# Kernel optimization log

Measured on AMD Instinct MI355X. Metric: run time of the kernel, lower is better.

## Reference

```python
import jax, jax.numpy as jnp
import numpy as np

D_MODEL = 1024
NUM_HEADS = 16
HEAD_DIM = D_MODEL // NUM_HEADS
B, S = 2, 2048


def setup_inputs() -> dict:
    key = jax.random.key(0)
    ks = jax.random.split(key, 10)
    sc = 1.0 / np.sqrt(D_MODEL)
    return {
        "x": jax.random.normal(ks[0], (B, S, D_MODEL), jnp.float32),
        "y": jax.random.normal(ks[1], (B, S, D_MODEL), jnp.float32),
        "Wkv": jax.random.normal(ks[2], (D_MODEL, 2 * D_MODEL), jnp.float32) * sc,
        "bkv": jax.random.normal(ks[3], (2 * D_MODEL,), jnp.float32) * 0.01,
        "Wq": jax.random.normal(ks[4], (D_MODEL, D_MODEL), jnp.float32) * sc,
        "bq": jax.random.normal(ks[5], (D_MODEL,), jnp.float32) * 0.01,
        "Wo": jax.random.normal(ks[6], (D_MODEL, D_MODEL), jnp.float32) * sc,
        "bo": jax.random.normal(ks[7], (D_MODEL,), jnp.float32) * 0.01,
    }


def reference(x, y, Wkv, bkv, Wq, bq, Wo, bo):
    b, s, d = x.shape
    # projections: kv from x (keys/values come from encoder side), q from y
    kv = x @ Wkv + bkv                      # [B, S, 2*d_model]
    q = y @ Wq + bq                         # [B, S, d_model]
    kv = kv.reshape(b, s, NUM_HEADS, 2 * HEAD_DIM).transpose(0, 2, 1, 3)  # [B,H,S,2*hd]
    q = q.reshape(b, s, NUM_HEADS, HEAD_DIM).transpose(0, 2, 1, 3)        # [B,H,S,hd]
    k, v = jnp.split(kv, 2, axis=-1)        # each [B,H,S,hd]
    scaled = jnp.einsum("bhqd,bhkd->bhqk", q, k) / np.sqrt(HEAD_DIM)      # [B,H,S,S]
    attention = jax.nn.softmax(scaled, axis=-1)
    values = jnp.einsum("bhqk,bhkd->bhqd", attention, v)                  # [B,H,S,hd]
    values = values.transpose(0, 2, 1, 3).reshape(b, s, d)                # [B,S,d_model]
    return values @ Wo + bo
```

## Files before the change

kernel.cpp:

```cpp
#include <hip/hip_runtime.h>
#include <hip/hip_bf16.h>

typedef __attribute__((ext_vector_type(8))) short short8;
typedef __attribute__((ext_vector_type(4))) short short4v;
typedef __attribute__((ext_vector_type(4))) float f32x4;

#define B_  2
#define S_  2048
#define H_  16
#define HD_ 64
#define D_  1024
#define QSCALE 0.18033688f

__device__ __forceinline__ short f2bs(float f) {
  union { float f; unsigned u; } c; c.f = f;
  unsigned u = c.u;
  u += 0x7fffu + ((u >> 16) & 1u);
  return (short)(u >> 16);
}

__device__ __forceinline__ float bs2f(short v) {
  union { unsigned u; float f; } c;
  c.u = ((unsigned)(unsigned short)v) << 16;
  return c.f;
}

__device__ __forceinline__ unsigned pack_bf16(float a, float b) {
  __hip_bfloat162 h = __float22bfloat162_rn(float2{a, b});
  return *reinterpret_cast<unsigned*>(&h);
}

__device__ __forceinline__ float fexp2(float x) {
#if __has_builtin(__builtin_amdgcn_exp2f)
  return __builtin_amdgcn_exp2f(x);
#else
  return exp2f(x);
#endif
}

__device__ __forceinline__ float frcp(float x) {
#if __has_builtin(__builtin_amdgcn_rcpf)
  return __builtin_amdgcn_rcpf(x);
#else
  return 1.0f / x;
#endif
}

#define GL2LDS(gp, lp) __builtin_amdgcn_global_load_lds( \
    (const __attribute__((address_space(1))) unsigned int*)(gp), \
    (__attribute__((address_space(3))) unsigned int*)(lp), 16, 0, 0)

__global__ __launch_bounds__(256)
void prep_kernel(const float* __restrict__ x, const float* __restrict__ y,
                 short* __restrict__ xb, short* __restrict__ yb,
                 const float* __restrict__ Wkv, short* __restrict__ Wkvt,
                 const float* __restrict__ Wq, short* __restrict__ Wqt,
                 const float* __restrict__ Wo, short* __restrict__ Wot) {
  __shared__ float tile[64][65];
  int bx = blockIdx.x;
  if (bx < 8192) {
    int i = bx * 256 + threadIdx.x;
    const float4* src; short4v* dst; int j;
    if (i < (1 << 20)) { src = (const float4*)x; dst = (short4v*)xb; j = i; }
    else               { src = (const float4*)y; dst = (short4v*)yb; j = i - (1 << 20); }
    float4 f = src[j];
    short4v o;
    o.x = f2bs(f.x); o.y = f2bs(f.y); o.z = f2bs(f.z); o.w = f2bs(f.w);
    dst[j] = o;
    return;
  }
  bx -= 8192;
  const float* in; short* out; int C, c0, r0;
  if (bx < 512)      { in = Wkv; out = Wkvt; C = 2048; c0 = (bx & 31) * 64; r0 = (bx >> 5) * 64; }
  else if (bx < 768) { bx -= 512; in = Wq; out = Wqt; C = 1024; c0 = (bx & 15) * 64; r0 = (bx >> 4) * 64; }
  else               { bx -= 768; in = Wo; out = Wot; C = 1024; c0 = (bx & 15) * 64; r0 = (bx >> 4) * 64; }
  const int tx = threadIdx.x & 63, ty = threadIdx.x >> 6;
#pragma unroll
  for (int i = 0; i < 16; ++i) {
    int r = ty + i * 4;
    tile[r][tx] = in[(size_t)(r0 + r) * C + c0 + tx];
  }
  __syncthreads();
#pragma unroll
  for (int i = 0; i < 16; ++i) {
    int r = ty + i * 4;
    out[(size_t)(c0 + r) * 1024 + r0 + tx] = f2bs(tile[tx][r]);
  }
}

template <int MODE>
__device__ __forceinline__ void gemm_body(const short* __restrict__ A, const short* __restrict__ Bt,
                                          const float* __restrict__ bias,
                                          void* __restrict__ out0, void* __restrict__ out1,
                                          int m0, int n0, int K, short* smem) {
  short* As = smem;
  short* Bs = smem + 4096;
  const int tid = threadIdx.x;
  const int w = tid >> 6, lane = tid & 63;
  const int q15 = lane & 15, quad = lane >> 4;
  const int wm = (w >> 1) * 64, wn = (w & 1) * 64;

  f32x4 acc[4][4];
#pragma unroll
  for (int i = 0; i < 4; ++i)
#pragma unroll
    for (int j = 0; j < 4; ++j) acc[i][j] = f32x4{0.f, 0.f, 0.f, 0.f};

  const int srow = w * 16 + (lane >> 2);
  const int gch  = (lane & 3) ^ ((lane >> 3) & 3);
  const short* Ag = A + (size_t)(m0 + srow) * K + gch * 8;
  const short* Bg = Bt + (size_t)(n0 + srow) * K + gch * 8;
  short* Al = As + srow * 32 + (lane & 3) * 8;
  short* Bl = Bs + srow * 32 + (lane & 3) * 8;

  for (int kt = 0; kt < K; kt += 32) {
    GL2LDS(Ag + kt,                  Al);
    GL2LDS(Ag + kt + (size_t)64 * K, Al + 64 * 32);
    GL2LDS(Bg + kt,                  Bl);
    GL2LDS(Bg + kt + (size_t)64 * K, Bl + 64 * 32);
    __syncthreads();
    short8 af[4], bf[4];
#pragma unroll
    for (int mi = 0; mi < 4; ++mi) {
      int rr = wm + mi * 16 + q15;
      af[mi] = *(const short8*)(As + rr * 32 + ((quad ^ ((rr >> 1) & 3)) * 8));
    }
#pragma unroll
    for (int ni = 0; ni < 4; ++ni) {
      int rr = wn + ni * 16 + q15;
      bf[ni] = *(const short8*)(Bs + rr * 32 + ((quad ^ ((rr >> 1) & 3)) * 8));
    }
#pragma unroll
    for (int mi = 0; mi < 4; ++mi)
#pragma unroll
      for (int ni = 0; ni < 4; ++ni)
        acc[mi][ni] = __builtin_amdgcn_mfma_f32_16x16x32_bf16(af[mi], bf[ni], acc[mi][ni], 0, 0, 0);
    __syncthreads();
  }

  if constexpr (MODE == 0) {
#pragma unroll
    for (int mi = 0; mi < 4; ++mi)
#pragma unroll
      for (int ni = 0; ni < 4; ++ni) {
        const int n = n0 + wn + ni * 16 + q15;
        const float bn = bias[n];
#pragma unroll
        for (int r = 0; r < 4; ++r) {
          const int m = m0 + wm + mi * 16 + quad * 4 + r;
          int b = m >> 11, s = m & 2047, hh = n >> 6, d = n & 63;
          ((short*)out0)[((size_t)((b * H_ + hh) * S_ + s) << 6) + d] = f2bs((acc[mi][ni][r] + bn) * QSCALE);
        }
      }
  } else {
    const int hh = n0 >> 7;
    const int bb = m0 >> 11;
    const size_t bh = (size_t)(bb * H_ + hh);
    const int s0 = m0 & 2047;
    if ((w & 1) == 0) {
#pragma unroll
      for (int mi = 0; mi < 4; ++mi)
#pragma unroll
        for (int ni = 0; ni < 4; ++ni) {
          const float bn = bias[n0 + ni * 16 + q15];
#pragma unroll
          for (int r = 0; r < 4; ++r) {
            const int s = s0 + wm + mi * 16 + quad * 4 + r;
            ((short*)out0)[((bh * S_ + s) << 6) + ni * 16 + q15] = f2bs(acc[mi][ni][r] + bn);
          }
        }
    } else {
      short* VT = smem;
#pragma unroll
      for (int mi = 0; mi < 4; ++mi)
#pragma unroll
        for (int ni = 0; ni < 4; ++ni) {
          const int d = ni * 16 + q15;
          const float bn = bias[n0 + 64 + ni * 16 + q15];
#pragma unroll
          for (int t = 0; t < 2; ++t) {
            const int chunk = (wm >> 1) + mi * 8 + quad * 2 + t;
            unsigned pk = pack_bf16(acc[mi][ni][2 * t] + bn, acc[mi][ni][2 * t + 1] + bn);
            *reinterpret_cast<unsigned*>(VT + d * 128 + ((chunk ^ (d & 15)) * 2)) = pk;
          }
        }
    }
    __syncthreads();
    {
      short* VT = smem;
      const int d = tid >> 2, t4 = tid & 3;
      unsigned vals[16];
#pragma unroll
      for (int c = 0; c < 16; ++c) {
        int chunk = t4 * 16 + c;
        vals[c] = *reinterpret_cast<unsigned*>(VT + d * 128 + ((chunk ^ (d & 15)) * 2));
      }
      uint4* dst = (uint4*)((short*)out1 + ((bh * HD_ + d) << 11) + s0 + t4 * 32);
      dst[0] = uint4{vals[0], vals[1], vals[2], vals[3]};
      dst[1] = uint4{vals[4], vals[5], vals[6], vals[7]};
      dst[2] = uint4{vals[8], vals[9], vals[10], vals[11]};
      dst[3] = uint4{vals[12], vals[13], vals[14], vals[15]};
    }
  }
}

__global__ __launch_bounds__(256)
void proj_kernel(const short* __restrict__ xb, const short* __restrict__ Wkvt,
                 const float* __restrict__ bkv, short* __restrict__ Kb, short* __restrict__ Vtb,
                 const short* __restrict__ yb, const short* __restrict__ Wqt,
                 const float* __restrict__ bq, short* __restrict__ Qb) {
  __shared__ __align__(16) short smem[8192];
  int bx = blockIdx.x;
  if (bx < 512)
    gemm_body<1>(xb, Wkvt, bkv, Kb, Vtb, (bx >> 4) * 128, (bx & 15) * 128, 1024, smem);
  else {
    bx -= 512;
    gemm_body<0>(yb, Wqt, bq, Qb, nullptr, (bx >> 3) * 128, (bx & 7) * 128, 1024, smem);
  }
}

__global__ __launch_bounds__(512, 4)
void gemm_o_kernel(const short* __restrict__ A, const short* __restrict__ Bt,
                   const float* __restrict__ bias, float* __restrict__ out) {
  __shared__ __align__(16) short lds[32768];
  const int tid = threadIdx.x;
  const int w = tid >> 6, lane = tid & 63;
  const int q15 = lane & 15, quad = lane >> 4;
  const int xw = q15 & 7;
  const int m0 = blockIdx.y * 128, n0 = blockIdx.x * 128;
  const int wr = (w >> 1) * 32, wc = (w & 1) * 64;

  f32x4 acc[2][4];
#pragma unroll
  for (int i = 0; i < 2; ++i)
#pragma unroll
    for (int j = 0; j < 4; ++j) acc[i][j] = f32x4{0.f, 0.f, 0.f, 0.f};

  const int srow = w * 8 + (lane >> 3);
  const int gch  = (lane & 7) ^ (srow & 7);
  const int loff = w * 512 + lane * 8;
  const short* Ag = A + (size_t)(m0 + srow) * 1024 + gch * 8;
  const short* Bg = Bt + (size_t)(n0 + srow) * 1024 + gch * 8;

  GL2LDS(Ag,             lds + loff);
  GL2LDS(Ag + 64 * 1024, lds + loff + 4096);
  GL2LDS(Bg,             lds + 16384 + loff);
  GL2LDS(Bg + 64 * 1024, lds + 16384 + loff + 4096);

  for (int kt = 0; kt < 16; ++kt) {
    __syncthreads();
    const short* Ac = lds + ((kt & 1) ? 8192 : 0);
    const short* Bc = lds + 16384 + ((kt & 1) ? 8192 : 0);
    if (kt < 15) {
      const short* a2 = Ag + (kt + 1) * 64;
      const short* b2 = Bg + (kt + 1) * 64;
      short* ad = lds + ((kt & 1) ? 0 : 8192) + loff;
      short* bd = lds + 16384 + ((kt & 1) ? 0 : 8192) + loff;
      GL2LDS(a2,             ad);
      GL2LDS(a2 + 64 * 1024, ad + 4096);
      GL2LDS(b2,             bd);
      GL2LDS(b2 + 64 * 1024, bd + 4096);
    }
    short8 af[2][2], bf[4][2];
#pragma unroll
    for (int mi = 0; mi < 2; ++mi)
#pragma unroll
      for (int kk = 0; kk < 2; ++kk)
        af[mi][kk] = *(const short8*)(Ac + (wr + mi * 16 + q15) * 64 + (((kk * 4 + quad) ^ xw) * 8));
#pragma unroll
    for (int ni = 0; ni < 4; ++ni)
#pragma unroll
      for (int kk = 0; kk < 2; ++kk)
        bf[ni][kk] = *(const short8*)(Bc + (wc + ni * 16 + q15) * 64 + (((kk * 4 + quad) ^ xw) * 8));
#pragma unroll
    for (int mi = 0; mi < 2; ++mi)
#pragma unroll
      for (int ni = 0; ni < 4; ++ni)
#pragma unroll
        for (int kk = 0; kk < 2; ++kk)
          acc[mi][ni] = __builtin_amdgcn_mfma_f32_16x16x32_bf16(af[mi][kk], bf[ni][kk], acc[mi][ni], 0, 0, 0);
  }

#pragma unroll
  for (int mi = 0; mi < 2; ++mi)
#pragma unroll
    for (int ni = 0; ni < 4; ++ni) {
      const int n = n0 + wc + ni * 16 + q15;
      const float bn = bias[n];
#pragma unroll
      for (int r = 0; r < 4; ++r) {
        const int m = m0 + wr + mi * 16 + quad * 4 + r;
        out[(size_t)m * 1024 + n] = acc[mi][ni][r] + bn;
      }
    }
}

__global__ __launch_bounds__(256, 2)
void attn_kernel(const short* __restrict__ Q, const short* __restrict__ K,
                 const short* __restrict__ Vt, short* __restrict__ Obase,
                 float* __restrict__ Ls) {
  __shared__ __align__(16) short lds[32768];
  short* PQ = lds + 16384;
  const int tid = threadIdx.x;
  const int w = tid >> 6, lane = tid & 63;
  const int q15 = lane & 15, quad = lane >> 4;
  const int xw = q15 & 7;
  const int bx = blockIdx.x;
  const int xcd = bx & 7, slot = bx >> 3;
  const int pg = slot >> 4, rest = slot & 15;
  const int half = rest >> 3, qt = rest & 7;
  const int pp = xcd * 4 + pg;
  const int h = pp & 15, b = pp >> 4;
  const size_t bh = (size_t)(b * H_ + h);
  const short* Qg = Q + bh * (S_ * HD_) + qt * (256 * HD_);
  const short* Kg = K + bh * (S_ * HD_);
  const short* Vg = Vt + bh * (HD_ * S_);

  const int srow = w * 8 + (lane >> 3);
  const int gch  = (lane & 7) ^ (srow & 7);
  const int loff = w * 512 + lane * 8;

  {
    const short* qg = Qg + srow * 64 + gch * 8;
#pragma unroll
    for (int t = 0; t < 8; ++t) GL2LDS(qg + t * 2048, PQ + loff + t * 2048);
  }
  const short* kg = Kg + srow * 64 + gch * 8;
  const short* vg = Vg + (size_t)srow * S_ + gch * 8;
  const int kt0 = half * 16;
  GL2LDS(kg + kt0 * 4096,          lds + loff);
  GL2LDS(kg + kt0 * 4096 + 2048,   lds + loff + 2048);
  GL2LDS(vg + kt0 * 64,                    lds + 8192 + loff);
  GL2LDS(vg + kt0 * 64 + (size_t)32 * S_,  lds + 8192 + loff + 2048);
  __syncthreads();

  short8 aq[4][2];
#pragma unroll
  for (int st = 0; st < 4; ++st)
#pragma unroll
    for (int kk = 0; kk < 2; ++kk)
      aq[st][kk] = *(const short8*)(PQ + (w * 64 + st * 16 + q15) * 64 + (((kk * 4 + quad) ^ xw) * 8));
  short* Psw = PQ + w * 4096;

  f32x4 oacc[4][4];
#pragma unroll
  for (int st = 0; st < 4; ++st)
#pragma unroll
    for (int ni = 0; ni < 4; ++ni) oacc[st][ni] = f32x4{0.f, 0.f, 0.f, 0.f};
  float lsum[4] = {0.f, 0.f, 0.f, 0.f};
  const f32x4 zz = {0.f, 0.f, 0.f, 0.f};

  for (int kt = 0; kt < 16; ++kt) {
    __syncthreads();
    const short* Kc = lds + ((kt & 1) ? 4096 : 0);
    const short* Vc = lds + 8192 + ((kt & 1) ? 4096 : 0);
    if (kt < 15) {
      const int kn = kt0 + kt + 1;
      short* kd = lds + ((kt & 1) ? 0 : 4096) + loff;
      short* vd = lds + 8192 + ((kt & 1) ? 0 : 4096) + loff;
      GL2LDS(kg + kn * 4096,          kd);
      GL2LDS(kg + kn * 4096 + 2048,   kd + 2048);
      GL2LDS(vg + kn * 64,                    vd);
      GL2LDS(vg + kn * 64 + (size_t)32 * S_,  vd + 2048);
    }

    short8 ka[4][2];
#pragma unroll
    for (int mi = 0; mi < 4; ++mi) {
      const short* kr = Kc + (mi * 16 + q15) * 64;
      ka[mi][0] = *(const short8*)(kr + ((quad ^ xw) * 8));
      ka[mi][1] = *(const short8*)(kr + (((quad + 4) ^ xw) * 8));
    }

#pragma unroll
    for (int st = 0; st < 4; ++st) {
      short* Pst = Psw + st * 1024;
#pragma unroll
      for (int mi = 0; mi < 4; ++mi) {
        f32x4 t = __builtin_amdgcn_mfma_f32_16x16x32_bf16(ka[mi][0], aq[st][0], zz, 0, 0, 0);
        f32x4 s = __builtin_amdgcn_mfma_f32_16x16x32_bf16(ka[mi][1], aq[st][1], t, 0, 0, 0);
        float p0 = fexp2(s[0]), p1 = fexp2(s[1]), p2 = fexp2(s[2]), p3 = fexp2(s[3]);
        lsum[st] += (p0 + p1) + (p2 + p3);
        uint2 pk;
        pk.x = pack_bf16(p0, p1);
        pk.y = pack_bf16(p2, p3);
        *reinterpret_cast<uint2*>(Pst + q15 * 64 + (((mi * 2 + (quad >> 1)) ^ xw) * 8) + (quad & 1) * 4) = pk;
      }
    }

    short8 ap[4][2];
#pragma unroll
    for (int st = 0; st < 4; ++st)
#pragma unroll
      for (int kk = 0; kk < 2; ++kk)
        ap[st][kk] = *(const short8*)(Psw + st * 1024 + q15 * 64 + (((kk * 4 + quad) ^ xw) * 8));
#pragma unroll
    for (int ni = 0; ni < 4; ++ni) {
      const short* vr = Vc + (ni * 16 + q15) * 64;
#pragma unroll
      for (int kk = 0; kk < 2; ++kk) {
        short8 bv = *(const short8*)(vr + (((kk * 4 + quad) ^ xw) * 8));
#pragma unroll
        for (int st = 0; st < 4; ++st)
          oacc[st][ni] = __builtin_amdgcn_mfma_f32_16x16x32_bf16(ap[st][kk], bv, oacc[st][ni], 0, 0, 0);
      }
    }
  }

  short* Op = Obase + (size_t)half * (4 << 20);
#pragma unroll
  for (int st = 0; st < 4; ++st) {
    float l = lsum[st];
    l += __shfl_xor(l, 16);
    l += __shfl_xor(l, 32);
    const int qrow = qt * 256 + w * 64 + st * 16;
    if (quad == 0)
      Ls[half * 65536 + (int)bh * 2048 + qrow + q15] = l;
#pragma unroll
    for (int ni = 0; ni < 4; ++ni) {
      const int col = h * HD_ + ni * 16 + q15;
#pragma unroll
      for (int r = 0; r < 4; ++r) {
        const int m = b * S_ + qrow + quad * 4 + r;
        Op[(size_t)m * D_ + col] = f2bs(oacc[st][ni][r]);
      }
    }
  }
}

__global__ __launch_bounds__(256)
void comb_kernel(const short* __restrict__ O0, const short* __restrict__ O1,
                 const float* __restrict__ Ls, short* __restrict__ AO) {
  int idx = blockIdx.x * 256 + threadIdx.x;
  int m = idx >> 7, seg = idx & 127;
  int b = m >> 11, s = m & 2047, h = seg >> 3;
  int li = (b * 16 + h) * 2048 + s;
  float inv = frcp(Ls[li] + Ls[65536 + li]);
  short8 a = *(const short8*)(O0 + (size_t)m * 1024 + seg * 8);
  short8 c = *(const short8*)(O1 + (size_t)m * 1024 + seg * 8);
  short8 o;
#pragma unroll
  for (int i = 0; i < 8; ++i)
    o[i] = f2bs((bs2f(a[i]) + bs2f(c[i])) * inv);
  *(short8*)(AO + (size_t)m * 1024 + seg * 8) = o;
}

extern "C" void kernel_launch(void* const* d_in, const int* in_sizes, int n_in,
                              void* d_out, int out_size, void* d_ws, size_t ws_size,
                              hipStream_t stream) {
  const float* x   = (const float*)d_in[0];
  const float* y   = (const float*)d_in[1];
  const float* Wkv = (const float*)d_in[2];
  const float* bkv = (const float*)d_in[3];
  const float* Wq  = (const float*)d_in[4];
  const float* bq  = (const float*)d_in[5];
  const float* Wo  = (const float*)d_in[6];
  const float* bo  = (const float*)d_in[7];
  float* out = (float*)d_out;

  short* xb   = (short*)d_ws;
  short* yb   = xb + (4 << 20);
  short* Wkvt = yb + (4 << 20);
  short* Wqt  = Wkvt + (2 << 20);
  short* Wot  = Wqt + (1 << 20);
  short* Kb   = Wot + (1 << 20);
  short* Vtb  = Kb + (4 << 20);
  short* Qb   = Vtb + (4 << 20);
  short* AOb  = Qb + (4 << 20);
  float* Ls   = (float*)Wkvt;

  prep_kernel<<<9216, 256, 0, stream>>>(x, y, xb, yb, Wkv, Wkvt, Wq, Wqt, Wo, Wot);
  proj_kernel<<<768, 256, 0, stream>>>(xb, Wkvt, bkv, Kb, Vtb, yb, Wqt, bq, Qb);
  attn_kernel<<<512, 256, 0, stream>>>(Qb, Kb, Vtb, xb, Ls);
  comb_kernel<<<2048, 256, 0, stream>>>(xb, yb, Ls, AOb);
  gemm_o_kernel<<<dim3(8, 32), 512, 0, stream>>>(AOb, Wot, bo, out);
}
```

Before: 219.0 us.

## Fuse split-KV combine into attention via atomic counter and double-buffer projection GEMM

The separate combine kernel is removed. Each attention block now increments a per-(batch,head,q-tile) counter, and whichever of the two KV-halves finishes second merges both partial outputs in place, normalizing by the summed row sums. The projection GEMM is rewritten to use 512 threads, BK=64 tiles and double-buffered global-to-LDS prefetch. This saves a launch and a round trip through the combined buffer, and overlaps loads with MFMA work. In exchange it relies on threadfence/atomic ordering and on the counter being reset inside prep_kernel.

```diff
diff --git a/kernel.cpp b/kernel.cpp
--- a/kernel.cpp
+++ b/kernel.cpp
@@ -55,10 +55,12 @@
                  short* __restrict__ xb, short* __restrict__ yb,
                  const float* __restrict__ Wkv, short* __restrict__ Wkvt,
                  const float* __restrict__ Wq, short* __restrict__ Wqt,
-                 const float* __restrict__ Wo, short* __restrict__ Wot) {
+                 const float* __restrict__ Wo, short* __restrict__ Wot,
+                 int* __restrict__ cnt) {
   __shared__ float tile[64][65];
   int bx = blockIdx.x;
   if (bx < 8192) {
+    if (bx == 0) cnt[threadIdx.x] = 0;
     int i = bx * 256 + threadIdx.x;
     const float4* src; short4v* dst; int j;
     if (i < (1 << 20)) { src = (const float4*)x; dst = (short4v*)xb; j = i; }
@@ -89,65 +91,78 @@
 }
 
 template <int MODE>
-__device__ __forceinline__ void gemm_body(const short* __restrict__ A, const short* __restrict__ Bt,
-                                          const float* __restrict__ bias,
-                                          void* __restrict__ out0, void* __restrict__ out1,
-                                          int m0, int n0, int K, short* smem) {
-  short* As = smem;
-  short* Bs = smem + 4096;
+__device__ __forceinline__ void gemm_body8(const short* __restrict__ A, const short* __restrict__ Bt,
+                                           const float* __restrict__ bias,
+                                           void* __restrict__ out0, void* __restrict__ out1,
+                                           int m0, int n0, int K, short* lds) {
   const int tid = threadIdx.x;
   const int w = tid >> 6, lane = tid & 63;
   const int q15 = lane & 15, quad = lane >> 4;
-  const int wm = (w >> 1) * 64, wn = (w & 1) * 64;
-
-  f32x4 acc[4][4];
-#pragma unroll
-  for (int i = 0; i < 4; ++i)
+  const int xw = q15 & 7;
+  const int wr = (w >> 1) * 32, wc = (w & 1) * 64;
+
+  f32x4 acc[2][4];
+#pragma unroll
+  for (int i = 0; i < 2; ++i)
 #pragma unroll
     for (int j = 0; j < 4; ++j) acc[i][j] = f32x4{0.f, 0.f, 0.f, 0.f};
 
-  const int srow = w * 16 + (lane >> 2);
-  const int gch  = (lane & 3) ^ ((lane >> 3) & 3);
+  const int srow = w * 8 + (lane >> 3);
+  const int gch  = (lane & 7) ^ (srow & 7);
+  const int loff = w * 512 + lane * 8;
   const short* Ag = A + (size_t)(m0 + srow) * K + gch * 8;
   const short* Bg = Bt + (size_t)(n0 + srow) * K + gch * 8;
-  short* Al = As + srow * 32 + (lane & 3) * 8;
-  short* Bl = Bs + srow * 32 + (lane & 3) * 8;
-
-  for (int kt = 0; kt < K; kt += 32) {
-    GL2LDS(Ag + kt,                  Al);
-    GL2LDS(Ag + kt + (size_t)64 * K, Al + 64 * 32);
-    GL2LDS(Bg + kt,                  Bl);
-    GL2LDS(Bg + kt + (size_t)64 * K, Bl + 64 * 32);
+
+  GL2LDS(Ag,                  lds + loff);
+  GL2LDS(Ag + (size_t)64 * K, lds + loff + 4096);
+  GL2LDS(Bg,                  lds + 16384 + loff);
+  GL2LDS(Bg + (size_t)64 * K, lds + 16384 + loff + 4096);
+
+  const int NK = K >> 6;
+  for (int kt = 0; kt < NK; ++kt) {
     __syncthreads();
-    short8 af[4], bf[4];
-#pragma unroll
-    for (int mi = 0; mi < 4; ++mi) {
-      int rr = wm + mi * 16 + q15;
-      af[mi] = *(const short8*)(As + rr * 32 + ((quad ^ ((rr >> 1) & 3)) * 8));
-    }
-#pragma unroll
-    for (int ni = 0; ni < 4; ++ni) {
-      int rr = wn + ni * 16 + q15;
-      bf[ni] = *(const short8*)(Bs + rr * 32 + ((quad ^ ((rr >> 1) & 3)) * 8));
-    }
-#pragma unroll
-    for (int mi = 0; mi < 4; ++mi)
+    const short* Ac = lds + ((kt & 1) ? 8192 : 0);
+    const short* Bc = lds + 16384 + ((kt & 1) ? 8192 : 0);
+    if (kt < NK - 1) {
+      const short* a2 = Ag + (kt + 1) * 64;
+      const short* b2 = Bg + (kt + 1) * 64;
+      short* ad = lds + ((kt & 1) ? 0 : 8192) + loff;
+      short* bd = lds + 16384 + ((kt & 1) ? 0 : 8192) + loff;
+      GL2LDS(a2,                  ad);
+      GL2LDS(a2 + (size_t)64 * K, ad + 4096);
+      GL2LDS(b2,                  bd);
+      GL2LDS(b2 + (size_t)64 * K, bd + 4096);
+    }
+    short8 af[2][2], bf[4][2];
+#pragma unroll
+    for (int mi = 0; mi < 2; ++mi)
+#pragma unroll
+      for (int kk = 0; kk < 2; ++kk)
+        af[mi][kk] = *(const short8*)(Ac + (wr + mi * 16 + q15) * 64 + (((kk * 4 + quad) ^ xw) * 8));
+#pragma unroll
+    for (int ni = 0; ni < 4; ++ni)
+#pragma unroll
+      for (int kk = 0; kk < 2; ++kk)
+        bf[ni][kk] = *(const short8*)(Bc + (wc + ni * 16 + q15) * 64 + (((kk * 4 + quad) ^ xw) * 8));
+#pragma unroll
+    for (int mi = 0; mi < 2; ++mi)
 #pragma unroll
       for (int ni = 0; ni < 4; ++ni)
-        acc[mi][ni] = __builtin_amdgcn_mfma_f32_16x16x32_bf16(af[mi], bf[ni], acc[mi][ni], 0, 0, 0);
-    __syncthreads();
+#pragma unroll
+        for (int kk = 0; kk < 2; ++kk)
+          acc[mi][ni] = __builtin_amdgcn_mfma_f32_16x16x32_bf16(af[mi][kk], bf[ni][kk], acc[mi][ni], 0, 0, 0);
   }
 
   if constexpr (MODE == 0) {
 #pragma unroll
-    for (int mi = 0; mi < 4; ++mi)
+    for (int mi = 0; mi < 2; ++mi)
 #pragma unroll
       for (int ni = 0; ni < 4; ++ni) {
-        const int n = n0 + wn + ni * 16 + q15;
+        const int n = n0 + wc + ni * 16 + q15;
         const float bn = bias[n];
 #pragma unroll
         for (int r = 0; r < 4; ++r) {
-          const int m = m0 + wm + mi * 16 + quad * 4 + r;
+          const int m = m0 + wr + mi * 16 + quad * 4 + r;
           int b = m >> 11, s = m & 2047, hh = n >> 6, d = n & 63;
           ((short*)out0)[((size_t)((b * H_ + hh) * S_ + s) << 6) + d] = f2bs((acc[mi][ni][r] + bn) * QSCALE);
         }
@@ -157,29 +172,30 @@
     const int bb = m0 >> 11;
     const size_t bh = (size_t)(bb * H_ + hh);
     const int s0 = m0 & 2047;
+    __syncthreads();
+    short* VT = lds;
     if ((w & 1) == 0) {
 #pragma unroll
-      for (int mi = 0; mi < 4; ++mi)
+      for (int mi = 0; mi < 2; ++mi)
 #pragma unroll
         for (int ni = 0; ni < 4; ++ni) {
           const float bn = bias[n0 + ni * 16 + q15];
 #pragma unroll
           for (int r = 0; r < 4; ++r) {
-            const int s = s0 + wm + mi * 16 + quad * 4 + r;
+            const int s = s0 + wr + mi * 16 + quad * 4 + r;
             ((short*)out0)[((bh * S_ + s) << 6) + ni * 16 + q15] = f2bs(acc[mi][ni][r] + bn);
           }
         }
     } else {
-      short* VT = smem;
-#pragma unroll
-      for (int mi = 0; mi < 4; ++mi)
+#pragma unroll
+      for (int mi = 0; mi < 2; ++mi)
 #pragma unroll
         for (int ni = 0; ni < 4; ++ni) {
           const int d = ni * 16 + q15;
-          const float bn = bias[n0 + 64 + ni * 16 + q15];
+          const float bn = bias[n0 + 64 + d];
 #pragma unroll
           for (int t = 0; t < 2; ++t) {
-            const int chunk = (wm >> 1) + mi * 8 + quad * 2 + t;
+            const int chunk = (wr >> 1) + mi * 8 + quad * 2 + t;
             unsigned pk = pack_bf16(acc[mi][ni][2 * t] + bn, acc[mi][ni][2 * t + 1] + bn);
             *reinterpret_cast<unsigned*>(VT + d * 128 + ((chunk ^ (d & 15)) * 2)) = pk;
           }
@@ -187,35 +203,32 @@
     }
     __syncthreads();
     {
-      short* VT = smem;
-      const int d = tid >> 2, t4 = tid & 3;
-      unsigned vals[16];
-#pragma unroll
-      for (int c = 0; c < 16; ++c) {
-        int chunk = t4 * 16 + c;
+      const int d = tid >> 3, t8 = tid & 7;
+      unsigned vals[8];
+#pragma unroll
+      for (int c = 0; c < 8; ++c) {
+        int chunk = t8 * 8 + c;
         vals[c] = *reinterpret_cast<unsigned*>(VT + d * 128 + ((chunk ^ (d & 15)) * 2));
       }
-      uint4* dst = (uint4*)((short*)out1 + ((bh * HD_ + d) << 11) + s0 + t4 * 32);
+      uint4* dst = (uint4*)((short*)out1 + ((bh * HD_ + d) << 11) + s0 + t8 * 16);
       dst[0] = uint4{vals[0], vals[1], vals[2], vals[3]};
       dst[1] = uint4{vals[4], vals[5], vals[6], vals[7]};
-      dst[2] = uint4{vals[8], vals[9], vals[10], vals[11]};
-      dst[3] = uint4{vals[12], vals[13], vals[14], vals[15]};
-    }
-  }
-}
-
-__global__ __launch_bounds__(256)
+    }
+  }
+}
+
+__global__ __launch_bounds__(512, 4)
 void proj_kernel(const short* __restrict__ xb, const short* __restrict__ Wkvt,
                  const float* __restrict__ bkv, short* __restrict__ Kb, short* __restrict__ Vtb,
                  const short* __restrict__ yb, const short* __restrict__ Wqt,
                  const float* __restrict__ bq, short* __restrict__ Qb) {
-  __shared__ __align__(16) short smem[8192];
+  __shared__ __align__(16) short lds[32768];
   int bx = blockIdx.x;
   if (bx < 512)
-    gemm_body<1>(xb, Wkvt, bkv, Kb, Vtb, (bx >> 4) * 128, (bx & 15) * 128, 1024, smem);
+    gemm_body8<1>(xb, Wkvt, bkv, Kb, Vtb, (bx >> 4) * 128, (bx & 15) * 128, 1024, lds);
   else {
     bx -= 512;
-    gemm_body<0>(yb, Wqt, bq, Qb, nullptr, (bx >> 3) * 128, (bx & 7) * 128, 1024, smem);
+    gemm_body8<0>(yb, Wqt, bq, Qb, nullptr, (bx >> 3) * 128, (bx & 7) * 128, 1024, lds);
   }
 }
 
@@ -298,8 +311,9 @@
 __global__ __launch_bounds__(256, 2)
 void attn_kernel(const short* __restrict__ Q, const short* __restrict__ K,
                  const short* __restrict__ Vt, short* __restrict__ Obase,
-                 float* __restrict__ Ls) {
+                 float* __restrict__ Ls, int* __restrict__ cnt) {
   __shared__ __align__(16) short lds[32768];
+  __shared__ int oldflag;
   short* PQ = lds + 16384;
   const int tid = threadIdx.x;
   const int w = tid >> 6, lane = tid & 63;
@@ -426,23 +440,30 @@
       }
     }
   }
-}
-
-__global__ __launch_bounds__(256)
-void comb_kernel(const short* __restrict__ O0, const short* __restrict__ O1,
-                 const float* __restrict__ Ls, short* __restrict__ AO) {
-  int idx = blockIdx.x * 256 + threadIdx.x;
-  int m = idx >> 7, seg = idx & 127;
-  int b = m >> 11, s = m & 2047, h = seg >> 3;
-  int li = (b * 16 + h) * 2048 + s;
-  float inv = frcp(Ls[li] + Ls[65536 + li]);
-  short8 a = *(const short8*)(O0 + (size_t)m * 1024 + seg * 8);
-  short8 c = *(const short8*)(O1 + (size_t)m * 1024 + seg * 8);
-  short8 o;
-#pragma unroll
-  for (int i = 0; i < 8; ++i)
-    o[i] = f2bs((bs2f(a[i]) + bs2f(c[i])) * inv);
-  *(short8*)(AO + (size_t)m * 1024 + seg * 8) = o;
+
+  __syncthreads();
+  if (tid == 0) {
+    __threadfence();
+    oldflag = atomicAdd(&cnt[pp * 8 + qt], 1);
+  }
+  __syncthreads();
+  if (oldflag == 1) {
+    __threadfence();
+    const int s = qt * 256 + tid;
+    const int li = (int)bh * 2048 + s;
+    const float inv = frcp(Ls[li] + Ls[65536 + li]);
+    const size_t base = ((size_t)(b * S_ + s) << 10) + h * HD_;
+    short8* p0 = (short8*)(Obase + base);
+    const short8* p1 = (const short8*)(Obase + (size_t)(4 << 20) + base);
+#pragma unroll
+    for (int c = 0; c < 8; ++c) {
+      short8 a = p0[c], e = p1[c];
+      short8 v;
+#pragma unroll
+      for (int i = 0; i < 8; ++i) v[i] = f2bs((bs2f(a[i]) + bs2f(e[i])) * inv);
+      p0[c] = v;
+    }
+  }
 }
 
 extern "C" void kernel_launch(void* const* d_in, const int* in_sizes, int n_in,
@@ -466,12 +487,12 @@
   short* Kb   = Wot + (1 << 20);
   short* Vtb  = Kb + (4 << 20);
   short* Qb   = Vtb + (4 << 20);
-  short* AOb  = Qb + (4 << 20);
-  float* Ls   = (float*)Wkvt;
-
-  prep_kernel<<<9216, 256, 0, stream>>>(x, y, xb, yb, Wkv, Wkvt, Wq, Wqt, Wo, Wot);
-  proj_kernel<<<768, 256, 0, stream>>>(xb, Wkvt, bkv, Kb, Vtb, yb, Wqt, bq, Qb);
-  attn_kernel<<<512, 256, 0, stream>>>(Qb, Kb, Vtb, xb, Ls);
-  comb_kernel<<<2048, 256, 0, stream>>>(xb, yb, Ls, AOb);
-  gemm_o_kernel<<<dim3(8, 32), 512, 0, stream>>>(AOb, Wot, bo, out);
-}
+  short* LsR  = Qb + (4 << 20);
+  float* Ls   = (float*)LsR;
+  int*   cnt  = (int*)(Ls + 131072);
+
+  prep_kernel<<<9216, 256, 0, stream>>>(x, y, xb, yb, Wkv, Wkvt, Wq, Wqt, Wo, Wot, cnt);
+  proj_kernel<<<768, 512, 0, stream>>>(xb, Wkvt, bkv, Kb, Vtb, yb, Wqt, bq, Qb);
+  attn_kernel<<<512, 256, 0, stream>>>(Qb, Kb, Vtb, xb, Ls, cnt);
+  gemm_o_kernel<<<dim3(8, 32), 512, 0, stream>>>(xb, Wot, bo, out);
+}
```

Result: slower. 253.4 us (+15.7%).
